# Kernel tuning notes

Hardware: AMD Instinct MI355X
Metric: run time of the kernel (lower is better)

Reference implementation:

```python
import jax, jax.numpy as jnp
import numpy as np

H, MEL, ATT, TXT = 1024, 80, 640, 640   # n_hidden, n_mel, n_attn_channels, n_text+n_speaker
T, TTXT = 600, 128


def setup_inputs() -> dict:
    key = jax.random.key(0)
    ks = jax.random.split(key, 20)
    def w(k, shape, s=0.02):
        return (jax.random.normal(k, shape) * s).astype(jnp.float32)
    return {
        "residual": jax.random.normal(ks[0], (T, 1, MEL), jnp.float32),
        "text": jax.random.normal(ks[1], (TTXT, 1, TXT), jnp.float32),
        # attention_lstm: LSTM(MEL -> H), 1 layer
        "Wih_a": w(ks[2], (4 * H, MEL)), "Whh_a": w(ks[3], (4 * H, H)),
        "bih_a": jnp.zeros(4 * H, jnp.float32), "bhh_a": jnp.zeros(4 * H, jnp.float32),
        # Attention: query/key/value projections + scoring vector v
        "Wq": w(ks[4], (ATT, H)), "Wk": w(ks[5], (ATT, TXT)), "Wv": w(ks[6], (ATT, TXT)),
        "v_w": w(ks[7], (ATT,)),
        # decoder lstm: LSTM(H+ATT -> H), 2 layers
        "Wih0": w(ks[8], (4 * H, H + ATT)), "Whh0": w(ks[9], (4 * H, H)),
        "bih0": jnp.zeros(4 * H, jnp.float32), "bhh0": jnp.zeros(4 * H, jnp.float32),
        "Wih1": w(ks[10], (4 * H, H)), "Whh1": w(ks[11], (4 * H, H)),
        "bih1": jnp.zeros(4 * H, jnp.float32), "bhh1": jnp.zeros(4 * H, jnp.float32),
        # DenseLayer: two tanh(Linear(H,H))
        "D0w": w(ks[12], (H, H)), "D0b": jnp.zeros(H, jnp.float32),
        "D1w": w(ks[13], (H, H)), "D1b": jnp.zeros(H, jnp.float32),
        # Conv1d(H, 2*MEL, kernel=1) == Linear
        "conv_w": w(ks[14], (2 * MEL, H)), "conv_b": jnp.zeros(2 * MEL, jnp.float32),
        # gate layer: Linear(H+ATT, 1)
        "gate_w": w(ks[15], (H + ATT,)), "gate_b": jnp.zeros((), jnp.float32),
    }


def lstm_cell(x, h, c, Wih, Whh, bih, bhh):
    # PyTorch gate order: i, f, g, o
    g = Wih @ x + bih + Whh @ h + bhh
    i, f, gg, o = jnp.split(g, 4)
    c2 = jax.nn.sigmoid(f) * c + jax.nn.sigmoid(i) * jnp.tanh(gg)
    return jax.nn.sigmoid(o) * jnp.tanh(c2), c2


def ar_back_step(residual, text, Wih_a, Whh_a, bih_a, bhh_a, Wq, Wk, Wv, v_w,
                 Wih0, Whh0, bih0, bhh0, Wih1, Whh1, bih1, bhh1,
                 D0w, D0b, D1w, D1b, conv_w, conv_b, gate_w, gate_b):
    res = residual[::-1, 0, :]            # AR_Back_Step flips time; batch=1 squeezed
    txt = text[:, 0, :]                   # [TTXT, TXT]
    K = txt @ Wk.T                        # [TTXT, ATT]  (keys constant over steps)
    V = txt @ Wv.T                        # [TTXT, ATT]
    z = jnp.zeros(H, jnp.float32)
    carry0 = (jnp.zeros(MEL, jnp.float32), z, z, z, z, z, z)

    def step(carry, r_t):
        out_prev, h, c, h0, c0, h1, c1 = carry
        # attention LSTM on previous output
        h, c = lstm_cell(out_prev, h, c, Wih_a, Whh_a, bih_a, bhh_a)
        # additive (Bahdanau-style) attention: v . tanh(q + K)
        q = Wq @ h                                   # [ATT]
        scores = jnp.tanh(q[None, :] + K) @ v_w      # [TTXT]
        attn = jax.nn.softmax(scores)
        ctx = attn @ V                               # [ATT]
        dec_in = jnp.concatenate([h, ctx])           # [H+ATT]
        # 2-layer decoder LSTM
        h0, c0 = lstm_cell(dec_in, h0, c0, Wih0, Whh0, bih0, bhh0)
        h1, c1 = lstm_cell(h0, h1, c1, Wih1, Whh1, bih1, bhh1)
        # DenseLayer (tanh MLP) then 1x1 conv
        d = jnp.tanh(D1w @ jnp.tanh(D0w @ h1 + D0b) + D1b)
        dec_out = conv_w @ d + conv_b                # [2*MEL]
        log_s, b = dec_out[:MEL], dec_out[MEL:]
        out = (r_t - b) / jnp.exp(log_s)             # affine coupling inverse
        gate = jax.nn.sigmoid(gate_w @ dec_in + gate_b)
        return (out, h, c, h0, c0, h1, c1), (out, gate)

    _, (outs, gates) = jax.lax.scan(step, carry0, res)
    total = outs[::-1][:, None, :]                   # flip back, restore batch dim
    return total, gates


def reference(residual, text, Wih_a, Whh_a, bih_a, bhh_a, Wq, Wk, Wv, v_w,
              Wih0, Whh0, bih0, bhh0, Wih1, Whh1, bih1, bhh1,
              D0w, D0b, D1w, D1b, conv_w, conv_b, gate_w, gate_b):
    return ar_back_step(residual, text, Wih_a, Whh_a, bih_a, bhh_a, Wq, Wk, Wv, v_w,
                        Wih0, Whh0, bih0, bhh0, Wih1, Whh1, bih1, bhh1,
                        D0w, D0b, D1w, D1b, conv_w, conv_b, gate_w, gate_b)
```

## Files before the change

kernel.cpp:

```cpp
#include <hip/hip_runtime.h>

#define NBLK 256
#define NTHR 1024

constexpr int H = 1024, MEL = 80, ATT = 640, TXTD = 640, T = 600, TTXT = 128;
constexpr int G4 = 4096, DIN = H + ATT;

constexpr int WS_K     = 0;
constexpr int WS_V     = WS_K + TTXT * ATT;
constexpr int WS_HBUF  = WS_V + TTXT * ATT;
constexpr int WS_H0BUF = WS_HBUF + 2 * H;
constexpr int WS_H1BUF = WS_H0BUF + 2 * H;
constexpr int WS_Q     = WS_H1BUF + 2 * H;
constexpr int WS_CTX   = WS_Q + ATT;
constexpr int WS_DEN   = WS_CTX + ATT;
constexpr int WS_GH    = WS_DEN + 1;
constexpr int WS_DEC   = (WS_GH + 1 + 15) & ~15;
constexpr int WS_A0    = (WS_DEC + 2 * MEL + 15) & ~15;
constexpr int WS_END   = WS_A0 + H;
constexpr int WS_BAR   = (WS_END + 63) & ~63;

constexpr int SM_W0  = 0;
constexpr int SM_H   = SM_W0 + 16 * DIN;
constexpr int SM_H0  = SM_H + H;
constexpr int SM_H1  = SM_H0 + H;
constexpr int SM_ATT = SM_H1 + H;
constexpr int SM_K   = SM_ATT + ATT;
constexpr int SM_V   = SM_K + ATT;
constexpr int SM_VW  = SM_V + ATT;
constexpr int SM_OUT = SM_VW + ATT;
constexpr int SM_DEC = SM_OUT + MEL;
constexpr int SM_RED = SM_DEC + 2 * MEL;
constexpr int SM_D   = SM_RED + 16;
constexpr int SM_DEN = SM_D + 4;
constexpr int SM_CNT = SM_DEN + 1;
constexpr size_t SM_BYTES = ((size_t)SM_CNT * 4 + 255) & ~(size_t)255;

#define KEEP4(v) \
  asm volatile("" : "+v"((v).x), "+v"((v).y), "+v"((v).z), "+v"((v).w))

struct Params {
  const float *residual, *text, *Wih_a, *Whh_a, *bih_a, *bhh_a,
      *Wq, *Wk, *Wv, *v_w, *Wih0, *Whh0, *bih0, *bhh0,
      *Wih1, *Whh1, *bih1, *bhh1, *D0w, *D0b, *D1w, *D1b,
      *conv_w, *conv_b, *gate_w, *gate_b;
  float* out;
  float* ws;
};

__device__ __forceinline__ float sigm(float x) { return 1.0f / (1.0f + __expf(-x)); }
__device__ __forceinline__ float ftanh(float x) {
  x = fminf(15.f, fmaxf(-15.f, x));
  float e = __expf(2.f * x);
  return (e - 1.f) / (e + 1.f);
}

__device__ __forceinline__ float aload(const float* p) {
  return __hip_atomic_load(p, __ATOMIC_RELAXED, __HIP_MEMORY_SCOPE_AGENT);
}
__device__ __forceinline__ void astore(float* p, float v) {
  __hip_atomic_store(p, v, __ATOMIC_RELAXED, __HIP_MEMORY_SCOPE_AGENT);
}

__device__ __forceinline__ void gbar(unsigned* bar, unsigned k) {
  asm volatile("s_waitcnt vmcnt(0)" ::: "memory");
  __syncthreads();
  if (threadIdx.x == 0) {
    unsigned* leaf = bar + (blockIdx.x & 15) * 32;
    unsigned o = __hip_atomic_fetch_add(leaf, 1u, __ATOMIC_RELAXED,
                                        __HIP_MEMORY_SCOPE_AGENT);
    if ((o & 15) == 15) {
      unsigned r = __hip_atomic_fetch_add(bar + 512, 1u, __ATOMIC_RELAXED,
                                          __HIP_MEMORY_SCOPE_AGENT);
      if ((r & 15) == 15)
        __hip_atomic_fetch_add(bar + 544, 1u, __ATOMIC_RELAXED,
                               __HIP_MEMORY_SCOPE_AGENT);
    }
    while (__hip_atomic_load(bar + 544, __ATOMIC_RELAXED,
                             __HIP_MEMORY_SCOPE_AGENT) < k)
      __builtin_amdgcn_s_sleep(1);
  }
  __syncthreads();
}

__device__ __forceinline__ float red64(float s) {
#pragma unroll
  for (int off = 32; off; off >>= 1) s += __shfl_xor(s, off, 64);
  return s;
}

__device__ __forceinline__ float dot16pin(float4 w0, float4 w1, float4 w2,
                                          float4 w3, const float* x, int lane) {
  const float4* x4 = (const float4*)x;
  float4 b0 = x4[lane], b1 = x4[lane + 64], b2 = x4[lane + 128],
         b3 = x4[lane + 192];
  float s0 = w0.x * b0.x, s1 = w1.x * b1.x;
  s0 = fmaf(w0.y, b0.y, s0); s1 = fmaf(w1.y, b1.y, s1);
  s0 = fmaf(w0.z, b0.z, s0); s1 = fmaf(w1.z, b1.z, s1);
  s0 = fmaf(w0.w, b0.w, s0); s1 = fmaf(w1.w, b1.w, s1);
  s0 = fmaf(w2.x, b2.x, s0); s1 = fmaf(w3.x, b3.x, s1);
  s0 = fmaf(w2.y, b2.y, s0); s1 = fmaf(w3.y, b3.y, s1);
  s0 = fmaf(w2.z, b2.z, s0); s1 = fmaf(w3.z, b3.z, s1);
  s0 = fmaf(w2.w, b2.w, s0); s1 = fmaf(w3.w, b3.w, s1);
  return s0 + s1;
}

__device__ __forceinline__ float dot16load(const float* w, const float* x,
                                           int lane) {
  const float4* w4 = (const float4*)w;
  const float4* x4 = (const float4*)x;
  float4 a0 = w4[lane], a1 = w4[lane + 64], a2 = w4[lane + 128],
         a3 = w4[lane + 192];
  float4 b0 = x4[lane], b1 = x4[lane + 64], b2 = x4[lane + 128],
         b3 = x4[lane + 192];
  float s0 = a0.x * b0.x, s1 = a1.x * b1.x;
  s0 = fmaf(a0.y, b0.y, s0); s1 = fmaf(a1.y, b1.y, s1);
  s0 = fmaf(a0.z, b0.z, s0); s1 = fmaf(a1.z, b1.z, s1);
  s0 = fmaf(a0.w, b0.w, s0); s1 = fmaf(a1.w, b1.w, s1);
  s0 = fmaf(a2.x, b2.x, s0); s1 = fmaf(a3.x, b3.x, s1);
  s0 = fmaf(a2.y, b2.y, s0); s1 = fmaf(a3.y, b3.y, s1);
  s0 = fmaf(a2.z, b2.z, s0); s1 = fmaf(a3.z, b3.z, s1);
  s0 = fmaf(a2.w, b2.w, s0); s1 = fmaf(a3.w, b3.w, s1);
  return s0 + s1;
}

__device__ __forceinline__ float wave_dot(const float* __restrict__ w,
                                          const float* __restrict__ x,
                                          int n4, int lane) {
  float s = 0.f;
  const float4* w4 = (const float4*)w;
  const float4* x4 = (const float4*)x;
  for (int i = lane; i < n4; i += 64) {
    float4 a = w4[i];
    float4 b = x4[i];
    s = fmaf(a.x, b.x, s);
    s = fmaf(a.y, b.y, s);
    s = fmaf(a.z, b.z, s);
    s = fmaf(a.w, b.w, s);
  }
  return red64(s);
}

__global__ void __launch_bounds__(NTHR, 4) ar_kernel(Params p) {
  const int b = blockIdx.x;
  const int tid = threadIdx.x;
  const int wave = tid >> 6;
  const int lane = tid & 63;
  const int sg = wave >> 2;
  const int wg = wave & 3;
  const int gw = b * 16 + wave;

  float* ws = p.ws;
  float* Kw = ws + WS_K;
  float* Vw = ws + WS_V;
  float* hbuf = ws + WS_HBUF;
  float* h0buf = ws + WS_H0BUF;
  float* h1buf = ws + WS_H1BUF;
  float* qv = ws + WS_Q;
  float* ctxa = ws + WS_CTX;
  float* den = ws + WS_DEN;
  float* ghp = ws + WS_GH;
  float* dec = ws + WS_DEC;
  float* a0 = ws + WS_A0;
  unsigned* bar = (unsigned*)(ws + WS_BAR);

  extern __shared__ __align__(16) float smem[];
  float* s_w0 = smem + SM_W0;
  float* s_h = smem + SM_H;
  float* s_h0 = smem + SM_H0;
  float* s_h1 = smem + SM_H1;
  float* s_att = smem + SM_ATT;
  float* s_k = smem + SM_K;
  float* s_v = smem + SM_V;
  float* s_vw = smem + SM_VW;
  float* s_out = smem + SM_OUT;
  float* s_dec = smem + SM_DEC;
  float* s_red = smem + SM_RED;
  float* s_d = smem + SM_D;
  float* s_den = smem + SM_DEN;

  const int e = 4 * b + sg;
  const int grow = e + wg * H;

  const float4* WA = (const float4*)(p.Whh_a + (size_t)grow * H);
  float4 wa0 = WA[lane], wa1 = WA[lane + 64], wa2 = WA[lane + 128],
         wa3 = WA[lane + 192];
  KEEP4(wa0); KEEP4(wa1); KEEP4(wa2); KEEP4(wa3);
  const float4* W0 = (const float4*)(p.Whh0 + (size_t)grow * H);
  float4 w00 = W0[lane], w01 = W0[lane + 64], w02 = W0[lane + 128],
         w03 = W0[lane + 192];
  KEEP4(w00); KEEP4(w01); KEEP4(w02); KEEP4(w03);
  const float4* W1 = (const float4*)(p.Whh1 + (size_t)grow * H);
  float4 w10 = W1[lane], w11 = W1[lane + 64], w12 = W1[lane + 128],
         w13 = W1[lane + 192];
  KEEP4(w10); KEEP4(w11); KEEP4(w12); KEEP4(w13);
  const float4* WI = (const float4*)(p.Wih1 + (size_t)grow * H);
  float4 wi0 = WI[lane], wi1 = WI[lane + 64], wi2 = WI[lane + 128],
         wi3 = WI[lane + 192];
  KEEP4(wi0); KEEP4(wi1); KEEP4(wi2); KEEP4(wi3);
  float4 wma = make_float4(0.f, 0.f, 0.f, 0.f);
  if (lane < MEL / 4)
    wma = ((const float4*)(p.Wih_a + (size_t)grow * MEL))[lane];
  KEEP4(wma);
  float4 wf = ((const float4*)(p.D0w + (size_t)e * H))[wg * 64 + lane];
  KEEP4(wf);
  float4 wgd = ((const float4*)(p.D1w + (size_t)e * H))[wg * 64 + lane];
  KEEP4(wgd);
  float4 wcv = make_float4(0.f, 0.f, 0.f, 0.f);
  if (tid < 2 * MEL) wcv = ((const float4*)(p.conv_w + (size_t)tid * H))[b];
  KEEP4(wcv);
  const float ba = p.bih_a[grow] + p.bhh_a[grow];
  const float b0s = p.bih0[grow] + p.bhh0[grow];
  const float b1s = p.bih1[grow] + p.bhh1[grow];

  const float* xsrc = nullptr;
  if (gw < ATT) xsrc = p.Wq + (size_t)gw * H;
  else if (gw == ATT) xsrc = p.gate_w;

  {
    const float4* src = (const float4*)(p.Wih0 + (size_t)grow * DIN);
    float4* dst = (float4*)(s_w0 + wave * DIN);
    for (int i = lane; i < DIN / 4; i += 64) dst[i] = src[i];
  }
  for (int i = tid; i < ATT; i += NTHR) s_vw[i] = p.v_w[i];

  float c_reg = 0.f, c0_reg = 0.f, c1_reg = 0.f;
  float u0_reg = 0.f, u1_reg = 0.f, w0h_reg = 0.f;

  unsigned bk = 0;

  if (b == 0) {
    for (int i = tid; i < 6 * H; i += NTHR) astore(&hbuf[i], 0.f);
  }
  for (int idx = gw; idx < 2 * TTXT * ATT; idx += NBLK * 16) {
    int isV = idx >= TTXT * ATT;
    int rem = isV ? idx - TTXT * ATT : idx;
    int j = rem / ATT;
    int a = rem - j * ATT;
    const float* wrow = (isV ? p.Wv : p.Wk) + a * TXTD;
    float s = wave_dot(wrow, p.text + j * TXTD, TXTD / 4, lane);
    if (lane == 0) astore(&(isV ? Vw : Kw)[j * ATT + a], s);
  }
  gbar(bar, ++bk);
  if (b < TTXT) {
    for (int i = tid; i < ATT; i += NTHR) {
      s_k[i] = aload(&Kw[b * ATT + i]);
      s_v[i] = aload(&Vw[b * ATT + i]);
    }
  }

  for (int t = 0; t < T; ++t) {
    const float* h_old = hbuf + (t & 1) * H;
    float* h_new = hbuf + ((t + 1) & 1) * H;
    const float* h0_old = h0buf + (t & 1) * H;
    float* h0_new = h0buf + ((t + 1) & 1) * H;
    const float* h1_old = h1buf + (t & 1) * H;
    float* h1_new = h1buf + ((t + 1) & 1) * H;

    s_h[tid] = aload(h_old + tid);
    s_h0[tid] = aload(h0_old + tid);
    s_h1[tid] = aload(h1_old + tid);
    if (tid < 2 * MEL) s_dec[tid] = aload(dec + tid);
    __syncthreads();
    if (tid < MEL) {
      float o = 0.f;
      if (t != 0) {
        float ls = s_dec[tid] + p.conv_b[tid];
        float bb = s_dec[MEL + tid] + p.conv_b[MEL + tid];
        float r = p.residual[(T - t) * MEL + tid];
        o = (r - bb) * __expf(-ls);
        if (b == 0) p.out[(T - t) * MEL + tid] = o;
      }
      s_out[tid] = o;
    }
    __syncthreads();
    {
      float pa = dot16pin(wa0, wa1, wa2, wa3, s_h, lane);
      if (lane < MEL / 4) {
        float4 bm = ((const float4*)s_out)[lane];
        pa = fmaf(wma.x, bm.x, pa);
        pa = fmaf(wma.y, bm.y, pa);
        pa = fmaf(wma.z, bm.z, pa);
        pa = fmaf(wma.w, bm.w, pa);
      }
      float pu0 = dot16pin(w00, w01, w02, w03, s_h0, lane);
      float pu1 = dot16pin(w10, w11, w12, w13, s_h1, lane);
      pa = red64(pa);
      u0_reg = red64(pu0);
      u1_reg = red64(pu1);
      if (lane == 0) s_red[wave] = pa + ba;
      __syncthreads();
      if (tid < 4) {
        int ee = 4 * b + tid;
        float gi = s_red[tid * 4 + 0], gf = s_red[tid * 4 + 1];
        float gg = s_red[tid * 4 + 2], go = s_red[tid * 4 + 3];
        float c2 = sigm(gf) * c_reg + sigm(gi) * ftanh(gg);
        c_reg = c2;
        astore(&h_new[ee], sigm(go) * ftanh(c2));
      }
    }
    gbar(bar, ++bk);

    s_h[tid] = aload(h_new + tid);
    __syncthreads();
    {
      float s0 = dot16load(s_w0 + wave * DIN, s_h, lane);
      w0h_reg = red64(s0);
      if (xsrc) {
        float q = dot16load(xsrc, s_h, lane);
        q = red64(q);
        if (lane == 0) {
          if (gw < ATT) astore(&qv[gw], q);
          else astore(&ghp[0], q);
        }
      }
      if (b == NBLK - 1) {
        for (int i = tid; i < ATT; i += NTHR) astore(&ctxa[i], 0.f);
        if (tid == 0) astore(den, 0.f);
        for (int i = tid; i < 2 * MEL; i += NTHR) astore(&dec[i], 0.f);
      }
    }
    gbar(bar, ++bk);

    if (b < TTXT) {
      if (tid < ATT) s_att[tid] = aload(&qv[tid]);
      __syncthreads();
      float sp = 0.f;
      for (int i = tid; i < ATT; i += NTHR)
        sp += ftanh(s_att[i] + s_k[i]) * s_vw[i];
      sp = red64(sp);
      if (lane == 0) s_red[wave] = sp;
      __syncthreads();
      float sc = 0.f;
#pragma unroll
      for (int k = 0; k < 16; ++k) sc += s_red[k];
      float pj = __expf(sc - 16.f);
      for (int i = tid; i < ATT; i += NTHR)
        atomicAdd(&ctxa[i], pj * s_v[i]);
      if (tid == 0) atomicAdd(den, pj);
    }
    gbar(bar, ++bk);

    {
      if (tid < ATT) s_att[tid] = aload(&ctxa[tid]);
      if (tid == NTHR - 1) s_den[0] = aload(den);
      __syncthreads();
      const float4* W4 = (const float4*)(s_w0 + wave * DIN + H);
      const float4* X4 = (const float4*)s_att;
      float4 a_ = W4[lane], b_ = X4[lane];
      float4 a2 = W4[lane + 64], b2 = X4[lane + 64];
      float s = a_.x * b_.x;
      s = fmaf(a_.y, b_.y, s); s = fmaf(a_.z, b_.z, s); s = fmaf(a_.w, b_.w, s);
      s = fmaf(a2.x, b2.x, s); s = fmaf(a2.y, b2.y, s);
      s = fmaf(a2.z, b2.z, s); s = fmaf(a2.w, b2.w, s);
      if (lane < 32) {
        float4 a3 = W4[128 + lane], b3 = X4[128 + lane];
        s = fmaf(a3.x, b3.x, s); s = fmaf(a3.y, b3.y, s);
        s = fmaf(a3.z, b3.z, s); s = fmaf(a3.w, b3.w, s);
      }
      s = red64(s);
      float inv = 1.f / s_den[0];
      if (lane == 0) s_red[wave] = s * inv + w0h_reg + u0_reg + b0s;
      if (b == 0 && wave == 15) {
        float gc = wave_dot(p.gate_w + H, s_att, ATT / 4, lane);
        if (lane == 0) {
          float gh = aload(&ghp[0]);
          p.out[T * MEL + t] = sigm(gh + gc * inv + p.gate_b[0]);
        }
      }
      __syncthreads();
      if (tid < 4) {
        int ee = 4 * b + tid;
        float gi = s_red[tid * 4 + 0], gf = s_red[tid * 4 + 1];
        float gg = s_red[tid * 4 + 2], go = s_red[tid * 4 + 3];
        float c2 = sigm(gf) * c0_reg + sigm(gi) * ftanh(gg);
        c0_reg = c2;
        astore(&h0_new[ee], sigm(go) * ftanh(c2));
      }
    }
    gbar(bar, ++bk);

    s_h[tid] = aload(h0_new + tid);
    __syncthreads();
    {
      float pe = dot16pin(wi0, wi1, wi2, wi3, s_h, lane);
      pe = red64(pe);
      if (lane == 0) s_red[wave] = pe + u1_reg + b1s;
      __syncthreads();
      if (tid < 4) {
        int ee = 4 * b + tid;
        float gi = s_red[tid * 4 + 0], gf = s_red[tid * 4 + 1];
        float gg = s_red[tid * 4 + 2], go = s_red[tid * 4 + 3];
        float c2 = sigm(gf) * c1_reg + sigm(gi) * ftanh(gg);
        c1_reg = c2;
        astore(&h1_new[ee], sigm(go) * ftanh(c2));
      }
    }
    gbar(bar, ++bk);

    s_h[tid] = aload(h1_new + tid);
    __syncthreads();
    {
      float4 x = ((const float4*)s_h)[wg * 64 + lane];
      float s = wf.x * x.x;
      s = fmaf(wf.y, x.y, s); s = fmaf(wf.z, x.z, s); s = fmaf(wf.w, x.w, s);
      s = red64(s);
      if (lane == 0) s_red[wave] = s;
      __syncthreads();
      if (tid < 4) {
        int r2 = 4 * b + tid;
        float tot = s_red[tid * 4] + s_red[tid * 4 + 1] + s_red[tid * 4 + 2] +
                    s_red[tid * 4 + 3];
        astore(&a0[r2], ftanh(tot + p.D0b[r2]));
      }
    }
    gbar(bar, ++bk);

    s_h[tid] = aload(a0 + tid);
    __syncthreads();
    {
      float4 x = ((const float4*)s_h)[wg * 64 + lane];
      float s = wgd.x * x.x;
      s = fmaf(wgd.y, x.y, s); s = fmaf(wgd.z, x.z, s); s = fmaf(wgd.w, x.w, s);
      s = red64(s);
      if (lane == 0) s_red[wave] = s;
      __syncthreads();
      if (tid < 4) {
        int r2 = 4 * b + tid;
        float tot = s_red[tid * 4] + s_red[tid * 4 + 1] + s_red[tid * 4 + 2] +
                    s_red[tid * 4 + 3];
        s_d[tid] = ftanh(tot + p.D1b[r2]);
      }
      __syncthreads();
      if (tid < 2 * MEL) {
        float acc = wcv.x * s_d[0];
        acc = fmaf(wcv.y, s_d[1], acc);
        acc = fmaf(wcv.z, s_d[2], acc);
        acc = fmaf(wcv.w, s_d[3], acc);
        atomicAdd(&dec[tid], acc);
      }
    }
    gbar(bar, ++bk);
  }

  if (b == 0 && tid < MEL) {
    float ls = aload(&dec[tid]) + p.conv_b[tid];
    float bb = aload(&dec[MEL + tid]) + p.conv_b[MEL + tid];
    float r = p.residual[tid];
    p.out[tid] = (r - bb) * __expf(-ls);
  }
}

extern "C" void kernel_launch(void* const* d_in, const int* in_sizes, int n_in,
                              void* d_out, int out_size, void* d_ws, size_t ws_size,
                              hipStream_t stream) {
  Params hp;
  hp.residual = (const float*)d_in[0];
  hp.text = (const float*)d_in[1];
  hp.Wih_a = (const float*)d_in[2];
  hp.Whh_a = (const float*)d_in[3];
  hp.bih_a = (const float*)d_in[4];
  hp.bhh_a = (const float*)d_in[5];
  hp.Wq = (const float*)d_in[6];
  hp.Wk = (const float*)d_in[7];
  hp.Wv = (const float*)d_in[8];
  hp.v_w = (const float*)d_in[9];
  hp.Wih0 = (const float*)d_in[10];
  hp.Whh0 = (const float*)d_in[11];
  hp.bih0 = (const float*)d_in[12];
  hp.bhh0 = (const float*)d_in[13];
  hp.Wih1 = (const float*)d_in[14];
  hp.Whh1 = (const float*)d_in[15];
  hp.bih1 = (const float*)d_in[16];
  hp.bhh1 = (const float*)d_in[17];
  hp.D0w = (const float*)d_in[18];
  hp.D0b = (const float*)d_in[19];
  hp.D1w = (const float*)d_in[20];
  hp.D1b = (const float*)d_in[21];
  hp.conv_w = (const float*)d_in[22];
  hp.conv_b = (const float*)d_in[23];
  hp.gate_w = (const float*)d_in[24];
  hp.gate_b = (const float*)d_in[25];
  hp.out = (float*)d_out;
  hp.ws = (float*)d_ws;

  hipMemsetAsync((char*)d_ws + (size_t)WS_BAR * sizeof(float), 0, 4096, stream);

  void* args[] = {&hp};
  hipLaunchCooperativeKernel((void*)ar_kernel, dim3(NBLK), dim3(NTHR), args,
                             (uint32_t)SM_BYTES, stream);
}
```

Measured before the change: 26.93 ms.

## Split grid barrier into arrive/wait and overlap recurrent matvecs with barrier waits

Result: faster. 26.20 ms (-2.7%).

```diff
diff --git a/kernel.cpp b/kernel.cpp
--- a/kernel.cpp
+++ b/kernel.cpp
@@ -8,10 +8,10 @@
 
 constexpr int WS_K     = 0;
 constexpr int WS_V     = WS_K + TTXT * ATT;
-constexpr int WS_HBUF  = WS_V + TTXT * ATT;
-constexpr int WS_H0BUF = WS_HBUF + 2 * H;
-constexpr int WS_H1BUF = WS_H0BUF + 2 * H;
-constexpr int WS_Q     = WS_H1BUF + 2 * H;
+constexpr int WS_HV    = WS_V + TTXT * ATT;
+constexpr int WS_H0V   = WS_HV + H;
+constexpr int WS_H1V   = WS_H0V + H;
+constexpr int WS_Q     = WS_H1V + H;
 constexpr int WS_CTX   = WS_Q + ATT;
 constexpr int WS_DEN   = WS_CTX + ATT;
 constexpr int WS_GH    = WS_DEN + 1;
@@ -24,7 +24,8 @@
 constexpr int SM_H   = SM_W0 + 16 * DIN;
 constexpr int SM_H0  = SM_H + H;
 constexpr int SM_H1  = SM_H0 + H;
-constexpr int SM_ATT = SM_H1 + H;
+constexpr int SM_A0  = SM_H1 + H;
+constexpr int SM_ATT = SM_A0 + H;
 constexpr int SM_K   = SM_ATT + ATT;
 constexpr int SM_V   = SM_K + ATT;
 constexpr int SM_VW  = SM_V + ATT;
@@ -62,22 +63,22 @@
   __hip_atomic_store(p, v, __ATOMIC_RELAXED, __HIP_MEMORY_SCOPE_AGENT);
 }
 
-__device__ __forceinline__ void gbar(unsigned* bar, unsigned k) {
+__device__ __forceinline__ void g_arrive(unsigned* bar) {
   asm volatile("s_waitcnt vmcnt(0)" ::: "memory");
   __syncthreads();
   if (threadIdx.x == 0) {
     unsigned* leaf = bar + (blockIdx.x & 15) * 32;
     unsigned o = __hip_atomic_fetch_add(leaf, 1u, __ATOMIC_RELAXED,
                                         __HIP_MEMORY_SCOPE_AGENT);
-    if ((o & 15) == 15) {
-      unsigned r = __hip_atomic_fetch_add(bar + 512, 1u, __ATOMIC_RELAXED,
-                                          __HIP_MEMORY_SCOPE_AGENT);
-      if ((r & 15) == 15)
-        __hip_atomic_fetch_add(bar + 544, 1u, __ATOMIC_RELAXED,
-                               __HIP_MEMORY_SCOPE_AGENT);
-    }
+    if ((o & 15) == 15)
+      __hip_atomic_fetch_add(bar + 544, 1u, __ATOMIC_RELAXED,
+                             __HIP_MEMORY_SCOPE_AGENT);
+  }
+}
+__device__ __forceinline__ void g_wait(unsigned* bar, unsigned target) {
+  if (threadIdx.x == 0) {
     while (__hip_atomic_load(bar + 544, __ATOMIC_RELAXED,
-                             __HIP_MEMORY_SCOPE_AGENT) < k)
+                             __HIP_MEMORY_SCOPE_AGENT) < target)
       __builtin_amdgcn_s_sleep(1);
   }
   __syncthreads();
@@ -153,15 +154,15 @@
   float* ws = p.ws;
   float* Kw = ws + WS_K;
   float* Vw = ws + WS_V;
-  float* hbuf = ws + WS_HBUF;
-  float* h0buf = ws + WS_H0BUF;
-  float* h1buf = ws + WS_H1BUF;
+  float* hv = ws + WS_HV;
+  float* h0v = ws + WS_H0V;
+  float* h1v = ws + WS_H1V;
   float* qv = ws + WS_Q;
   float* ctxa = ws + WS_CTX;
   float* den = ws + WS_DEN;
   float* ghp = ws + WS_GH;
   float* dec = ws + WS_DEC;
-  float* a0 = ws + WS_A0;
+  float* a0g = ws + WS_A0;
   unsigned* bar = (unsigned*)(ws + WS_BAR);
 
   extern __shared__ __align__(16) float smem[];
@@ -169,6 +170,7 @@
   float* s_h = smem + SM_H;
   float* s_h0 = smem + SM_H0;
   float* s_h1 = smem + SM_H1;
+  float* s_a0 = smem + SM_A0;
   float* s_att = smem + SM_ATT;
   float* s_k = smem + SM_K;
   float* s_v = smem + SM_V;
@@ -223,15 +225,15 @@
     for (int i = lane; i < DIN / 4; i += 64) dst[i] = src[i];
   }
   for (int i = tid; i < ATT; i += NTHR) s_vw[i] = p.v_w[i];
+  s_h[tid] = 0.f;
+  s_h0[tid] = 0.f;
+  s_h1[tid] = 0.f;
 
   float c_reg = 0.f, c0_reg = 0.f, c1_reg = 0.f;
   float u0_reg = 0.f, u1_reg = 0.f, w0h_reg = 0.f;
 
   unsigned bk = 0;
 
-  if (b == 0) {
-    for (int i = tid; i < 6 * H; i += NTHR) astore(&hbuf[i], 0.f);
-  }
   for (int idx = gw; idx < 2 * TTXT * ATT; idx += NBLK * 16) {
     int isV = idx >= TTXT * ATT;
     int rem = isV ? idx - TTXT * ATT : idx;
@@ -241,7 +243,7 @@
     float s = wave_dot(wrow, p.text + j * TXTD, TXTD / 4, lane);
     if (lane == 0) astore(&(isV ? Vw : Kw)[j * ATT + a], s);
   }
-  gbar(bar, ++bk);
+  g_arrive(bar); ++bk; g_wait(bar, 16 * bk);
   if (b < TTXT) {
     for (int i = tid; i < ATT; i += NTHR) {
       s_k[i] = aload(&Kw[b * ATT + i]);
@@ -250,16 +252,6 @@
   }
 
   for (int t = 0; t < T; ++t) {
-    const float* h_old = hbuf + (t & 1) * H;
-    float* h_new = hbuf + ((t + 1) & 1) * H;
-    const float* h0_old = h0buf + (t & 1) * H;
-    float* h0_new = h0buf + ((t + 1) & 1) * H;
-    const float* h1_old = h1buf + (t & 1) * H;
-    float* h1_new = h1buf + ((t + 1) & 1) * H;
-
-    s_h[tid] = aload(h_old + tid);
-    s_h0[tid] = aload(h0_old + tid);
-    s_h1[tid] = aload(h1_old + tid);
     if (tid < 2 * MEL) s_dec[tid] = aload(dec + tid);
     __syncthreads();
     if (tid < MEL) {
@@ -283,11 +275,7 @@
         pa = fmaf(wma.z, bm.z, pa);
         pa = fmaf(wma.w, bm.w, pa);
       }
-      float pu0 = dot16pin(w00, w01, w02, w03, s_h0, lane);
-      float pu1 = dot16pin(w10, w11, w12, w13, s_h1, lane);
       pa = red64(pa);
-      u0_reg = red64(pu0);
-      u1_reg = red64(pu1);
       if (lane == 0) s_red[wave] = pa + ba;
       __syncthreads();
       if (tid < 4) {
@@ -296,31 +284,30 @@
         float gg = s_red[tid * 4 + 2], go = s_red[tid * 4 + 3];
         float c2 = sigm(gf) * c_reg + sigm(gi) * ftanh(gg);
         c_reg = c2;
-        astore(&h_new[ee], sigm(go) * ftanh(c2));
-      }
-    }
-    gbar(bar, ++bk);
-
-    s_h[tid] = aload(h_new + tid);
-    __syncthreads();
-    {
-      float s0 = dot16load(s_w0 + wave * DIN, s_h, lane);
-      w0h_reg = red64(s0);
-      if (xsrc) {
-        float q = dot16load(xsrc, s_h, lane);
-        q = red64(q);
-        if (lane == 0) {
-          if (gw < ATT) astore(&qv[gw], q);
-          else astore(&ghp[0], q);
-        }
-      }
-      if (b == NBLK - 1) {
-        for (int i = tid; i < ATT; i += NTHR) astore(&ctxa[i], 0.f);
-        if (tid == 0) astore(den, 0.f);
-        for (int i = tid; i < 2 * MEL; i += NTHR) astore(&dec[i], 0.f);
-      }
-    }
-    gbar(bar, ++bk);
+        astore(&hv[ee], sigm(go) * ftanh(c2));
+      }
+    }
+    g_arrive(bar); ++bk;
+    g_wait(bar, 16 * bk);
+
+    s_h[tid] = aload(hv + tid);
+    __syncthreads();
+    if (xsrc) {
+      float q = dot16load(xsrc, s_h, lane);
+      q = red64(q);
+      if (lane == 0) {
+        if (gw < ATT) astore(&qv[gw], q);
+        else astore(&ghp[0], q);
+      }
+    }
+    if (b == NBLK - 1) {
+      for (int i = tid; i < ATT; i += NTHR) astore(&ctxa[i], 0.f);
+      if (tid == 0) astore(den, 0.f);
+      for (int i = tid; i < 2 * MEL; i += NTHR) astore(&dec[i], 0.f);
+    }
+    g_arrive(bar); ++bk;
+    w0h_reg = red64(dot16load(s_w0 + wave * DIN, s_h, lane));
+    g_wait(bar, 16 * bk);
 
     if (b < TTXT) {
       if (tid < ATT) s_att[tid] = aload(&qv[tid]);
@@ -339,7 +326,8 @@
         atomicAdd(&ctxa[i], pj * s_v[i]);
       if (tid == 0) atomicAdd(den, pj);
     }
-    gbar(bar, ++bk);
+    g_arrive(bar); ++bk;
+    g_wait(bar, 16 * bk);
 
     {
       if (tid < ATT) s_att[tid] = aload(&ctxa[tid]);
@@ -361,13 +349,6 @@
       s = red64(s);
       float inv = 1.f / s_den[0];
       if (lane == 0) s_red[wave] = s * inv + w0h_reg + u0_reg + b0s;
-      if (b == 0 && wave == 15) {
-        float gc = wave_dot(p.gate_w + H, s_att, ATT / 4, lane);
-        if (lane == 0) {
-          float gh = aload(&ghp[0]);
-          p.out[T * MEL + t] = sigm(gh + gc * inv + p.gate_b[0]);
-        }
-      }
       __syncthreads();
       if (tid < 4) {
         int ee = 4 * b + tid;
@@ -375,15 +356,24 @@
         float gg = s_red[tid * 4 + 2], go = s_red[tid * 4 + 3];
         float c2 = sigm(gf) * c0_reg + sigm(gi) * ftanh(gg);
         c0_reg = c2;
-        astore(&h0_new[ee], sigm(go) * ftanh(c2));
-      }
-    }
-    gbar(bar, ++bk);
-
-    s_h[tid] = aload(h0_new + tid);
+        astore(&h0v[ee], sigm(go) * ftanh(c2));
+      }
+    }
+    g_arrive(bar); ++bk;
+    if (b == 0 && wave == 15) {
+      float inv = 1.f / s_den[0];
+      float gc = wave_dot(p.gate_w + H, s_att, ATT / 4, lane);
+      if (lane == 0) {
+        float gh = aload(&ghp[0]);
+        p.out[T * MEL + t] = sigm(gh + gc * inv + p.gate_b[0]);
+      }
+    }
+    g_wait(bar, 16 * bk);
+
+    s_h0[tid] = aload(h0v + tid);
     __syncthreads();
     {
-      float pe = dot16pin(wi0, wi1, wi2, wi3, s_h, lane);
+      float pe = dot16pin(wi0, wi1, wi2, wi3, s_h0, lane);
       pe = red64(pe);
       if (lane == 0) s_red[wave] = pe + u1_reg + b1s;
       __syncthreads();
@@ -393,15 +383,17 @@
         float gg = s_red[tid * 4 + 2], go = s_red[tid * 4 + 3];
         float c2 = sigm(gf) * c1_reg + sigm(gi) * ftanh(gg);
         c1_reg = c2;
-        astore(&h1_new[ee], sigm(go) * ftanh(c2));
-      }
-    }
-    gbar(bar, ++bk);
-
-    s_h[tid] = aload(h1_new + tid);
+        astore(&h1v[ee], sigm(go) * ftanh(c2));
+      }
+    }
+    g_arrive(bar); ++bk;
+    u0_reg = red64(dot16pin(w00, w01, w02, w03, s_h0, lane));
+    g_wait(bar, 16 * bk);
+
+    s_h1[tid] = aload(h1v + tid);
     __syncthreads();
     {
-      float4 x = ((const float4*)s_h)[wg * 64 + lane];
+      float4 x = ((const float4*)s_h1)[wg * 64 + lane];
       float s = wf.x * x.x;
       s = fmaf(wf.y, x.y, s); s = fmaf(wf.z, x.z, s); s = fmaf(wf.w, x.w, s);
       s = red64(s);
@@ -411,15 +403,17 @@
         int r2 = 4 * b + tid;
         float tot = s_red[tid * 4] + s_red[tid * 4 + 1] + s_red[tid * 4 + 2] +
                     s_red[tid * 4 + 3];
-        astore(&a0[r2], ftanh(tot + p.D0b[r2]));
-      }
-    }
-    gbar(bar, ++bk);
-
-    s_h[tid] = aload(a0 + tid);
+        astore(&a0g[r2], ftanh(tot + p.D0b[r2]));
+      }
+    }
+    g_arrive(bar); ++bk;
+    u1_reg = red64(dot16pin(w10, w11, w12, w13, s_h1, lane));
+    g_wait(bar, 16 * bk);
+
+    s_a0[tid] = aload(a0g + tid);
     __syncthreads();
     {
-      float4 x = ((const float4*)s_h)[wg * 64 + lane];
+      float4 x = ((const float4*)s_a0)[wg * 64 + lane];
       float s = wgd.x * x.x;
       s = fmaf(wgd.y, x.y, s); s = fmaf(wgd.z, x.z, s); s = fmaf(wgd.w, x.w, s);
       s = red64(s);
@@ -440,7 +434,8 @@
         atomicAdd(&dec[tid], acc);
       }
     }
-    gbar(bar, ++bk);
+    g_arrive(bar); ++bk;
+    g_wait(bar, 16 * bk);
   }
 
   if (b == 0 && tid < MEL) {
```
